# Optimization experiments

Hardware: AMD Instinct MI355X
Metric: run time of the kernel (lower is better)

The kernel has to match this reference:

```python
import jax, jax.numpy as jnp
import numpy as np

B, D, L, K = 8192, 768, 16384, 100
EPS = 1e-5

def setup_inputs() -> dict:
    key = jax.random.key(0)
    k1, k2, k3, k4, k5 = jax.random.split(key, 5)
    x = jax.random.normal(k1, (B, D), jnp.float32)
    W_enc = jax.random.normal(k2, (D, L), jnp.float32) / np.float32(np.sqrt(D))
    W_dec = jax.random.normal(k3, (L, D), jnp.float32) / np.float32(np.sqrt(L))
    pre_bias = jax.random.normal(k4, (D,), jnp.float32) * 0.01
    latent_bias = jax.random.normal(k5, (L,), jnp.float32) * 0.01
    return {"x": x, "pre_bias": pre_bias, "latent_bias": latent_bias,
            "W_enc": W_enc, "W_dec": W_dec}

def reference(x, pre_bias, latent_bias, W_enc, W_dec):
    # normalize per-sample over the feature dim
    mu = jnp.mean(x, axis=-1, keepdims=True)                 # [B,1]
    std = jnp.std(x, axis=-1, keepdims=True)                 # [B,1]
    xn = (x - mu) / (std + EPS)                              # [B,D]
    # dense encode with bias-subtract fused
    latents_pre_act = (xn - pre_bias) @ W_enc + latent_bias  # [B,L]
    # top-k sparsification: keep k largest pre-activations, zero rest
    topk_vals, topk_idx = jax.lax.top_k(latents_pre_act, K)  # [B,K]
    rows = jnp.arange(latents_pre_act.shape[0])[:, None]     # [B,1]
    latents = jnp.zeros_like(latents_pre_act).at[rows, topk_idx].set(topk_vals)
    # sparse decode (dense GEMM on mostly-zero latents) + denormalize
    recons = latents @ W_dec + pre_bias                      # [B,D]
    recons = recons * std + mu
    return (latents_pre_act, latents, recons)
```

## Files before the change

kernel.cpp:

```cpp
#include <hip/hip_runtime.h>
#include <hip/hip_bf16.h>


#define Bdim 8192
#define Ddim 768
#define Ldim 16384
#define Kdim 100
#define BAND_W 1.5e-4f
#define BAND_MAX 64

typedef short s16x8 __attribute__((ext_vector_type(8)));
typedef float f32x4 __attribute__((ext_vector_type(4)));

__device__ inline float key2float(unsigned int k) {
  unsigned int u = (k & 0x80000000u) ? (k & 0x7fffffffu) : ~k;
  return __uint_as_float(u);
}

__global__ __launch_bounds__(256) void normalize_kernel(
    const float* __restrict__ x, const float* __restrict__ pre_bias,
    __hip_bfloat16* __restrict__ xh, __hip_bfloat16* __restrict__ xl,
    float* __restrict__ xn32, float* __restrict__ mu_out, float* __restrict__ std_out) {
  const int r = blockIdx.x, t = threadIdx.x;
  const int lane = t & 63, wid = t >> 6;
  const float* xr = x + (size_t)r * Ddim;
  float v0 = xr[t], v1 = xr[t + 256], v2 = xr[t + 512];
  __shared__ float sred[4];
  float s = v0 + v1 + v2;
  for (int off = 32; off > 0; off >>= 1) s += __shfl_down(s, off, 64);
  if (lane == 0) sred[wid] = s;
  __syncthreads();
  float mu = (sred[0] + sred[1] + sred[2] + sred[3]) * (1.0f / 768.0f);
  __syncthreads();
  float d0 = v0 - mu, d1 = v1 - mu, d2 = v2 - mu;
  s = d0 * d0 + d1 * d1 + d2 * d2;
  for (int off = 32; off > 0; off >>= 1) s += __shfl_down(s, off, 64);
  if (lane == 0) sred[wid] = s;
  __syncthreads();
  float var = (sred[0] + sred[1] + sred[2] + sred[3]) * (1.0f / 768.0f);
  float sd = sqrtf(var);
  float inv = 1.0f / (sd + 1e-5f);
  size_t base = (size_t)r * Ddim;
  #pragma unroll
  for (int j = 0; j < 3; ++j) {
    int c = t + j * 256;
    float d = (j == 0 ? d0 : (j == 1 ? d1 : d2));
    float sn = d * inv - pre_bias[c];
    __hip_bfloat16 hi = __float2bfloat16(sn);
    float lo = sn - __bfloat162float(hi);
    xn32[base + c] = sn;
    xh[base + c] = hi;
    xl[base + c] = __float2bfloat16(lo);
  }
  if (t == 0) { mu_out[r] = mu; std_out[r] = sd; }
}

__global__ __launch_bounds__(256) void wsplit_kernel(
    const float* __restrict__ W, __hip_bfloat16* __restrict__ Wh,
    __hip_bfloat16* __restrict__ Wl, float* __restrict__ Wt32) {
  __shared__ float tile[32][33];
  const int tx = threadIdx.x & 31, ty = threadIdx.x >> 5;
  const int l0 = blockIdx.x * 32, d0 = blockIdx.y * 32;
  #pragma unroll
  for (int i = ty; i < 32; i += 8)
    tile[i][tx] = W[(size_t)(d0 + i) * Ldim + l0 + tx];
  __syncthreads();
  #pragma unroll
  for (int i = ty; i < 32; i += 8) {
    float v = tile[tx][i];
    __hip_bfloat16 h = __float2bfloat16(v);
    float lo = v - __bfloat162float(h);
    const size_t off = (size_t)(l0 + i) * Ddim + d0 + tx;
    Wh[off] = h;
    Wl[off] = __float2bfloat16(lo);
    Wt32[off] = v;
  }
}

__global__ __launch_bounds__(256, 2) void encode_gemm_kernel(
    const __hip_bfloat16* __restrict__ xh, const __hip_bfloat16* __restrict__ xl,
    const __hip_bfloat16* __restrict__ wh, const __hip_bfloat16* __restrict__ wl,
    const float* __restrict__ lb, float* __restrict__ out0) {
  __shared__ __align__(16) __hip_bfloat16 sAh[128 * 32];
  __shared__ __align__(16) __hip_bfloat16 sAl[128 * 32];
  __shared__ __align__(16) __hip_bfloat16 sBh[128 * 32];
  __shared__ __align__(16) __hip_bfloat16 sBl[128 * 32];
  const int t = threadIdx.x;
  const int wid = t >> 6, lane = t & 63;
  const int quad = lane >> 4, lr = lane & 15;
  const int m0 = blockIdx.y * 128, n0 = blockIdx.x * 128;
  const int wm = (wid >> 1) * 64, wn = (wid & 1) * 64;

  f32x4 acc[4][4];
  #pragma unroll
  for (int i = 0; i < 4; ++i)
    #pragma unroll
    for (int j = 0; j < 4; ++j) acc[i][j] = (f32x4){0.f, 0.f, 0.f, 0.f};

  const int srow = lane >> 2;
  const int scol = (lane & 3) * 8;

  for (int kt = 0; kt < Ddim / 32; ++kt) {
    const int k0 = kt * 32;
    #pragma unroll
    for (int j = 0; j < 2; ++j) {
      const int c = wid * 2 + j;
      const int row = c * 16 + srow;
      const __hip_bfloat16* ga = xh + (size_t)(m0 + row) * Ddim + k0 + scol;
      const __hip_bfloat16* gb = xl + (size_t)(m0 + row) * Ddim + k0 + scol;
      const __hip_bfloat16* gc = wh + (size_t)(n0 + row) * Ddim + k0 + scol;
      const __hip_bfloat16* gd = wl + (size_t)(n0 + row) * Ddim + k0 + scol;
      __builtin_amdgcn_global_load_lds(
          (const __attribute__((address_space(1))) void*)ga,
          (__attribute__((address_space(3))) void*)(sAh + c * 512), 16, 0, 0);
      __builtin_amdgcn_global_load_lds(
          (const __attribute__((address_space(1))) void*)gb,
          (__attribute__((address_space(3))) void*)(sAl + c * 512), 16, 0, 0);
      __builtin_amdgcn_global_load_lds(
          (const __attribute__((address_space(1))) void*)gc,
          (__attribute__((address_space(3))) void*)(sBh + c * 512), 16, 0, 0);
      __builtin_amdgcn_global_load_lds(
          (const __attribute__((address_space(1))) void*)gd,
          (__attribute__((address_space(3))) void*)(sBl + c * 512), 16, 0, 0);
    }
    asm volatile("s_waitcnt vmcnt(0)" ::: "memory");
    __syncthreads();

    const int koff = quad * 8;
    s16x8 ah[4], al[4], bh[4], bl[4];
    #pragma unroll
    for (int nt = 0; nt < 4; ++nt) {
      bh[nt] = *(const s16x8*)&sBh[(wn + nt * 16 + lr) * 32 + koff];
      bl[nt] = *(const s16x8*)&sBl[(wn + nt * 16 + lr) * 32 + koff];
    }
    #pragma unroll
    for (int mt = 0; mt < 4; ++mt) {
      ah[mt] = *(const s16x8*)&sAh[(wm + mt * 16 + lr) * 32 + koff];
      al[mt] = *(const s16x8*)&sAl[(wm + mt * 16 + lr) * 32 + koff];
    }
    #pragma unroll
    for (int mt = 0; mt < 4; ++mt)
      #pragma unroll
      for (int nt = 0; nt < 4; ++nt) {
        acc[mt][nt] = __builtin_amdgcn_mfma_f32_16x16x32_bf16(
            ah[mt], bh[nt], acc[mt][nt], 0, 0, 0);
        acc[mt][nt] = __builtin_amdgcn_mfma_f32_16x16x32_bf16(
            al[mt], bh[nt], acc[mt][nt], 0, 0, 0);
        acc[mt][nt] = __builtin_amdgcn_mfma_f32_16x16x32_bf16(
            ah[mt], bl[nt], acc[mt][nt], 0, 0, 0);
      }
    __syncthreads();
  }

  #pragma unroll
  for (int nt = 0; nt < 4; ++nt) {
    const int n = n0 + wn + nt * 16 + lr;
    const float bias = lb[n];
    #pragma unroll
    for (int mt = 0; mt < 4; ++mt) {
      const int mbase = m0 + wm + mt * 16 + quad * 4;
      #pragma unroll
      for (int rg = 0; rg < 4; ++rg)
        out0[(size_t)(mbase + rg) * Ldim + n] = acc[mt][nt][rg] + bias;
    }
  }
}

__global__ __launch_bounds__(256) void topk_decode_kernel(
    const float* __restrict__ pre, const float* __restrict__ xn32,
    const float* __restrict__ Wt32, const float* __restrict__ lb,
    const float* __restrict__ Wdec, const float* __restrict__ pre_bias,
    const float* __restrict__ mu_arr, const float* __restrict__ std_arr,
    float* __restrict__ out_lat, float* __restrict__ out_rec) {
  const int r = blockIdx.x, t = threadIdx.x;
  const int lane = t & 63, wid = t >> 6;
  const float* row = pre + (size_t)r * Ldim;

  unsigned int keys[64];
  #pragma unroll
  for (int j = 0; j < 64; ++j) {
    unsigned int u = __float_as_uint(row[t + j * 256]);
    keys[j] = (u & 0x80000000u) ? ~u : (u | 0x80000000u);
  }

  __shared__ int sred[4];
  __shared__ int s_gt, s_band;
  __shared__ int sel_idx[128];
  __shared__ float sel_val[128];
  __shared__ int band_idx[BAND_MAX];
  __shared__ double band_rv[BAND_MAX];
  __shared__ float band_ov[BAND_MAX];
  __shared__ float sxn[Ddim];

  unsigned int kth = 0u;
  for (int bit = 31; bit >= 0; --bit) {
    const unsigned int cand = kth | (1u << bit);
    int c = 0;
    #pragma unroll
    for (int j = 0; j < 64; ++j) c += (keys[j] >= cand) ? 1 : 0;
    for (int off = 32; off > 0; off >>= 1) c += __shfl_down(c, off, 64);
    if (lane == 0) sred[wid] = c;
    __syncthreads();
    const int tot = sred[0] + sred[1] + sred[2] + sred[3];
    __syncthreads();
    if (tot >= Kdim) kth = cand;
  }

  const float kv = key2float(kth);
  const float Thi = kv + BAND_W, Tlo = kv - BAND_W;

  if (t == 0) { s_gt = 0; s_band = 0; }
  sxn[t] = xn32[(size_t)r * Ddim + t];
  sxn[t + 256] = xn32[(size_t)r * Ddim + t + 256];
  sxn[t + 512] = xn32[(size_t)r * Ddim + t + 512];
  __syncthreads();

  #pragma unroll
  for (int j = 0; j < 64; ++j) {
    const float v = key2float(keys[j]);
    if (v > Thi) {
      const int p = atomicAdd(&s_gt, 1);
      sel_idx[p] = t + j * 256;
      sel_val[p] = v;
    } else if (v >= Tlo) {
      const int p = atomicAdd(&s_band, 1);
      if (p < BAND_MAX) band_idx[p] = t + j * 256;
    }
  }
  __syncthreads();

  const int A = s_gt;
  const int m = min(s_band, BAND_MAX);
  const int need = Kdim - A;

  for (int c = wid; c < m; c += 4) {
    const int ci = band_idx[c];
    const float* wr = Wt32 + (size_t)ci * Ddim;
    double s = 0.0;
    #pragma unroll
    for (int j = 0; j < 12; ++j) {
      const int e = lane + j * 64;
      s += (double)sxn[e] * (double)wr[e];
    }
    for (int off = 32; off > 0; off >>= 1) s += __shfl_down(s, off, 64);
    if (lane == 0) {
      band_rv[c] = s + (double)lb[ci];
      band_ov[c] = (float)s + lb[ci];
    }
  }
  __syncthreads();

  if (t < m) {
    const double mine = band_rv[t];
    const int myi = band_idx[t];
    int rank = 0;
    for (int j = 0; j < m; ++j) {
      if (band_rv[j] > mine || (band_rv[j] == mine && band_idx[j] < myi)) ++rank;
    }
    if (rank < need) {
      const int p = atomicAdd(&s_gt, 1);
      sel_idx[p] = myi;
      sel_val[p] = band_ov[t];
    }
  }
  __syncthreads();

  float* lat = out_lat + (size_t)r * Ldim;
  float4 z; z.x = 0.f; z.y = 0.f; z.z = 0.f; z.w = 0.f;
  float4* lp = (float4*)lat;
  #pragma unroll
  for (int j = 0; j < 16; ++j) lp[t + j * 256] = z;
  __syncthreads();
  if (t < Kdim) lat[sel_idx[t]] = sel_val[t];

  float a0 = 0.f, a1 = 0.f, a2 = 0.f;
  for (int j = 0; j < Kdim; ++j) {
    const float v = sel_val[j];
    const float* wr = Wdec + (size_t)sel_idx[j] * Ddim;
    a0 += v * wr[t];
    a1 += v * wr[t + 256];
    a2 += v * wr[t + 512];
  }
  const float sd = std_arr[r], mv = mu_arr[r];
  float* rec = out_rec + (size_t)r * Ddim;
  rec[t]       = (a0 + pre_bias[t]) * sd + mv;
  rec[t + 256] = (a1 + pre_bias[t + 256]) * sd + mv;
  rec[t + 512] = (a2 + pre_bias[t + 512]) * sd + mv;
}

extern "C" void kernel_launch(void* const* d_in, const int* in_sizes, int n_in,
                              void* d_out, int out_size, void* d_ws, size_t ws_size,
                              hipStream_t stream) {
  const float* x     = (const float*)d_in[0];
  const float* pre_b = (const float*)d_in[1];
  const float* lat_b = (const float*)d_in[2];
  const float* W_enc = (const float*)d_in[3];
  const float* W_dec = (const float*)d_in[4];

  float* out0 = (float*)d_out;
  float* out1 = out0 + (size_t)Bdim * Ldim;
  float* out2 = out1 + (size_t)Bdim * Ldim;

  char* p = (char*)d_ws;
  __hip_bfloat16* xh = (__hip_bfloat16*)p; p += (size_t)Bdim * Ddim * 2;
  __hip_bfloat16* xl = (__hip_bfloat16*)p; p += (size_t)Bdim * Ddim * 2;
  __hip_bfloat16* Wh = (__hip_bfloat16*)p; p += (size_t)Ldim * Ddim * 2;
  __hip_bfloat16* Wl = (__hip_bfloat16*)p; p += (size_t)Ldim * Ddim * 2;
  float* xn32 = (float*)p;                 p += (size_t)Bdim * Ddim * 4;
  float* Wt32 = (float*)p;                 p += (size_t)Ldim * Ddim * 4;
  float* muv  = (float*)p;                 p += (size_t)Bdim * 4;
  float* sdv  = (float*)p;

  normalize_kernel<<<Bdim, 256, 0, stream>>>(x, pre_b, xh, xl, xn32, muv, sdv);
  wsplit_kernel<<<dim3(Ldim / 32, Ddim / 32), 256, 0, stream>>>(W_enc, Wh, Wl, Wt32);
  encode_gemm_kernel<<<dim3(Ldim / 128, Bdim / 128), 256, 0, stream>>>(
      xh, xl, Wh, Wl, lat_b, out0);
  topk_decode_kernel<<<Bdim, 256, 0, stream>>>(
      out0, xn32, Wt32, lat_b, W_dec, pre_b, muv, sdv, out1, out2);
}
```

Before: 2.062 ms.

## Enlarge encode GEMM tiles to 256x256 with double-buffered LDS and block swizzle

The encode GEMM moves from 128x128 tiles with 4 waves to 256x256 tiles with 8 waves. Each wave now owns a 128x64 subtile. LDS is double-buffered so the next k-slice loads asynchronously while MFMAs run on the current one, and the compute phases raise wave priority with s_setprio. Block indices are swizzled to improve L2 reuse. The goal is more operand reuse per byte loaded and hiding load latency, at the cost of 128KB of LDS and higher register pressure (128 accumulator floats per lane), which may limit occupancy to one block per CU despite the launch bound of 2.

```diff
diff --git a/kernel.cpp b/kernel.cpp
--- a/kernel.cpp
+++ b/kernel.cpp
@@ -77,91 +77,115 @@
   }
 }
 
-__global__ __launch_bounds__(256, 2) void encode_gemm_kernel(
+
+#define GLL(gp, lp)                                                         \
+  __builtin_amdgcn_global_load_lds(                                         \
+      (const __attribute__((address_space(1))) void*)(gp),                  \
+      (__attribute__((address_space(3))) void*)(lp), 16, 0, 0)
+
+#define MFMA_BF16 __builtin_amdgcn_mfma_f32_16x16x32_bf16
+
+#define STAGE(kt, dAh, dAl, dBh, dBl) do {                                  \
+    const size_t ko_ = (size_t)(kt) * 32;                                   \
+    GLL(gA0 + ko_,             (dAh) + (wid * 2) * 512);                    \
+    GLL(gA0 + ko_ + 16 * Ddim, (dAh) + (wid * 2 + 1) * 512);                \
+    GLL(gA1 + ko_,             (dAl) + (wid * 2) * 512);                    \
+    GLL(gA1 + ko_ + 16 * Ddim, (dAl) + (wid * 2 + 1) * 512);                \
+    GLL(gB0 + ko_,             (dBh) + (wid * 2) * 512);                    \
+    GLL(gB0 + ko_ + 16 * Ddim, (dBh) + (wid * 2 + 1) * 512);                \
+    GLL(gB1 + ko_,             (dBl) + (wid * 2) * 512);                    \
+    GLL(gB1 + ko_ + 16 * Ddim, (dBl) + (wid * 2 + 1) * 512);                \
+  } while (0)
+
+#define COMPUTE(dAh, dAl, dBh, dBl) do {                                    \
+    s16x8 bh_[4], bl_[4];                                                   \
+    _Pragma("unroll") for (int nt = 0; nt < 4; ++nt) {                      \
+      const int rb_ = (wc * 64 + nt * 16 + lr) * 32 + koff;                 \
+      bh_[nt] = *(const s16x8*)&(dBh)[rb_];                                 \
+      bl_[nt] = *(const s16x8*)&(dBl)[rb_];                                 \
+    }                                                                       \
+    _Pragma("unroll") for (int ph = 0; ph < 4; ++ph) {                      \
+      const int r0_ = (wr * 128 + ph * 32 + lr) * 32 + koff;                \
+      const int r1_ = r0_ + 16 * 32;                                        \
+      s16x8 a0h_ = *(const s16x8*)&(dAh)[r0_];                              \
+      s16x8 a0l_ = *(const s16x8*)&(dAl)[r0_];                              \
+      s16x8 a1h_ = *(const s16x8*)&(dAh)[r1_];                              \
+      s16x8 a1l_ = *(const s16x8*)&(dAl)[r1_];                              \
+      __builtin_amdgcn_s_setprio(1);                                        \
+      _Pragma("unroll") for (int nt = 0; nt < 4; ++nt) {                    \
+        acc[2*ph][nt]   = MFMA_BF16(a0h_, bh_[nt], acc[2*ph][nt], 0, 0, 0); \
+        acc[2*ph][nt]   = MFMA_BF16(a0l_, bh_[nt], acc[2*ph][nt], 0, 0, 0); \
+        acc[2*ph][nt]   = MFMA_BF16(a0h_, bl_[nt], acc[2*ph][nt], 0, 0, 0); \
+        acc[2*ph+1][nt] = MFMA_BF16(a1h_, bh_[nt], acc[2*ph+1][nt], 0, 0, 0);\
+        acc[2*ph+1][nt] = MFMA_BF16(a1l_, bh_[nt], acc[2*ph+1][nt], 0, 0, 0);\
+        acc[2*ph+1][nt] = MFMA_BF16(a1h_, bl_[nt], acc[2*ph+1][nt], 0, 0, 0);\
+      }                                                                     \
+      __builtin_amdgcn_s_setprio(0);                                        \
+    }                                                                       \
+  } while (0)
+
+__global__ __launch_bounds__(512, 2) void encode_gemm_kernel(
     const __hip_bfloat16* __restrict__ xh, const __hip_bfloat16* __restrict__ xl,
     const __hip_bfloat16* __restrict__ wh, const __hip_bfloat16* __restrict__ wl,
     const float* __restrict__ lb, float* __restrict__ out0) {
-  __shared__ __align__(16) __hip_bfloat16 sAh[128 * 32];
-  __shared__ __align__(16) __hip_bfloat16 sAl[128 * 32];
-  __shared__ __align__(16) __hip_bfloat16 sBh[128 * 32];
-  __shared__ __align__(16) __hip_bfloat16 sBl[128 * 32];
+  __shared__ __align__(16) __hip_bfloat16 sAh0[8192];
+  __shared__ __align__(16) __hip_bfloat16 sAl0[8192];
+  __shared__ __align__(16) __hip_bfloat16 sBh0[8192];
+  __shared__ __align__(16) __hip_bfloat16 sBl0[8192];
+  __shared__ __align__(16) __hip_bfloat16 sAh1[8192];
+  __shared__ __align__(16) __hip_bfloat16 sAl1[8192];
+  __shared__ __align__(16) __hip_bfloat16 sBh1[8192];
+  __shared__ __align__(16) __hip_bfloat16 sBl1[8192];
+
   const int t = threadIdx.x;
   const int wid = t >> 6, lane = t & 63;
-  const int quad = lane >> 4, lr = lane & 15;
-  const int m0 = blockIdx.y * 128, n0 = blockIdx.x * 128;
-  const int wm = (wid >> 1) * 64, wn = (wid & 1) * 64;
-
-  f32x4 acc[4][4];
-  #pragma unroll
-  for (int i = 0; i < 4; ++i)
+  const int lr = lane & 15, quad = lane >> 4;
+  const int koff = quad * 8;
+  const int wr = wid >> 2, wc = wid & 3;
+
+  const int flat = blockIdx.y * 64 + blockIdx.x;
+  const int swz = (flat & 7) * 256 + (flat >> 3);
+  const int m0 = (swz >> 6) * 256;
+  const int n0 = (swz & 63) * 256;
+
+  const int srow = lane >> 2, scol = (lane & 3) * 8;
+  const __hip_bfloat16* gA0 = xh + (size_t)(m0 + wid * 32 + srow) * Ddim + scol;
+  const __hip_bfloat16* gA1 = xl + (size_t)(m0 + wid * 32 + srow) * Ddim + scol;
+  const __hip_bfloat16* gB0 = wh + (size_t)(n0 + wid * 32 + srow) * Ddim + scol;
+  const __hip_bfloat16* gB1 = wl + (size_t)(n0 + wid * 32 + srow) * Ddim + scol;
+
+  f32x4 acc[8][4];
+  #pragma unroll
+  for (int i = 0; i < 8; ++i)
     #pragma unroll
     for (int j = 0; j < 4; ++j) acc[i][j] = (f32x4){0.f, 0.f, 0.f, 0.f};
 
-  const int srow = lane >> 2;
-  const int scol = (lane & 3) * 8;
-
-  for (int kt = 0; kt < Ddim / 32; ++kt) {
-    const int k0 = kt * 32;
-    #pragma unroll
-    for (int j = 0; j < 2; ++j) {
-      const int c = wid * 2 + j;
-      const int row = c * 16 + srow;
-      const __hip_bfloat16* ga = xh + (size_t)(m0 + row) * Ddim + k0 + scol;
-      const __hip_bfloat16* gb = xl + (size_t)(m0 + row) * Ddim + k0 + scol;
-      const __hip_bfloat16* gc = wh + (size_t)(n0 + row) * Ddim + k0 + scol;
-      const __hip_bfloat16* gd = wl + (size_t)(n0 + row) * Ddim + k0 + scol;
-      __builtin_amdgcn_global_load_lds(
-          (const __attribute__((address_space(1))) void*)ga,
-          (__attribute__((address_space(3))) void*)(sAh + c * 512), 16, 0, 0);
-      __builtin_amdgcn_global_load_lds(
-          (const __attribute__((address_space(1))) void*)gb,
-          (__attribute__((address_space(3))) void*)(sAl + c * 512), 16, 0, 0);
-      __builtin_amdgcn_global_load_lds(
-          (const __attribute__((address_space(1))) void*)gc,
-          (__attribute__((address_space(3))) void*)(sBh + c * 512), 16, 0, 0);
-      __builtin_amdgcn_global_load_lds(
-          (const __attribute__((address_space(1))) void*)gd,
-          (__attribute__((address_space(3))) void*)(sBl + c * 512), 16, 0, 0);
-    }
+  STAGE(0, sAh0, sAl0, sBh0, sBl0);
+  asm volatile("s_waitcnt vmcnt(0)" ::: "memory");
+  __builtin_amdgcn_s_barrier();
+
+  #pragma unroll 1
+  for (int kt = 0; kt < Ddim / 32; kt += 2) {
+    STAGE(kt + 1, sAh1, sAl1, sBh1, sBl1);
+    COMPUTE(sAh0, sAl0, sBh0, sBl0);
     asm volatile("s_waitcnt vmcnt(0)" ::: "memory");
-    __syncthreads();
-
-    const int koff = quad * 8;
-    s16x8 ah[4], al[4], bh[4], bl[4];
-    #pragma unroll
-    for (int nt = 0; nt < 4; ++nt) {
-      bh[nt] = *(const s16x8*)&sBh[(wn + nt * 16 + lr) * 32 + koff];
-      bl[nt] = *(const s16x8*)&sBl[(wn + nt * 16 + lr) * 32 + koff];
-    }
-    #pragma unroll
-    for (int mt = 0; mt < 4; ++mt) {
-      ah[mt] = *(const s16x8*)&sAh[(wm + mt * 16 + lr) * 32 + koff];
-      al[mt] = *(const s16x8*)&sAl[(wm + mt * 16 + lr) * 32 + koff];
-    }
-    #pragma unroll
-    for (int mt = 0; mt < 4; ++mt)
-      #pragma unroll
-      for (int nt = 0; nt < 4; ++nt) {
-        acc[mt][nt] = __builtin_amdgcn_mfma_f32_16x16x32_bf16(
-            ah[mt], bh[nt], acc[mt][nt], 0, 0, 0);
-        acc[mt][nt] = __builtin_amdgcn_mfma_f32_16x16x32_bf16(
-            al[mt], bh[nt], acc[mt][nt], 0, 0, 0);
-        acc[mt][nt] = __builtin_amdgcn_mfma_f32_16x16x32_bf16(
-            ah[mt], bl[nt], acc[mt][nt], 0, 0, 0);
-      }
-    __syncthreads();
+    __builtin_amdgcn_s_barrier();
+    if (kt + 2 < Ddim / 32) STAGE(kt + 2, sAh0, sAl0, sBh0, sBl0);
+    COMPUTE(sAh1, sAl1, sBh1, sBl1);
+    asm volatile("s_waitcnt vmcnt(0)" ::: "memory");
+    __builtin_amdgcn_s_barrier();
   }
 
   #pragma unroll
   for (int nt = 0; nt < 4; ++nt) {
-    const int n = n0 + wn + nt * 16 + lr;
+    const int n = n0 + wc * 64 + nt * 16 + lr;
     const float bias = lb[n];
     #pragma unroll
-    for (int mt = 0; mt < 4; ++mt) {
-      const int mbase = m0 + wm + mt * 16 + quad * 4;
+    for (int mt = 0; mt < 8; ++mt) {
+      const int mb = m0 + wr * 128 + mt * 16 + quad * 4;
       #pragma unroll
       for (int rg = 0; rg < 4; ++rg)
-        out0[(size_t)(mbase + rg) * Ldim + n] = acc[mt][nt][rg] + bias;
+        out0[(size_t)(mb + rg) * Ldim + n] = acc[mt][nt][rg] + bias;
     }
   }
 }
@@ -313,7 +337,7 @@
 
   normalize_kernel<<<Bdim, 256, 0, stream>>>(x, pre_b, xh, xl, xn32, muv, sdv);
   wsplit_kernel<<<dim3(Ldim / 32, Ddim / 32), 256, 0, stream>>>(W_enc, Wh, Wl, Wt32);
-  encode_gemm_kernel<<<dim3(Ldim / 128, Bdim / 128), 256, 0, stream>>>(
+  encode_gemm_kernel<<<dim3(Ldim / 256, Bdim / 256), 512, 0, stream>>>(
       xh, xl, Wh, Wl, lat_b, out0);
   topk_decode_kernel<<<Bdim, 256, 0, stream>>>(
       out0, xn32, Wt32, lat_b, W_dec, pre_b, muv, sdv, out1, out2);
```

Measured after the change: 2.048 ms. Within noise of the previous version (-0.6%).
